# Kernel optimization log

Hardware: AMD Instinct MI355X
Metric: run time of the kernel (lower is better)

## Reference

```python
import jax, jax.numpy as jnp
import numpy as np

B, L, DM, H = 2, 2048, 1024, 16
D = DM // H  # head_dim = key_dim = 64


def setup_inputs() -> dict:
    key = jax.random.key(0)
    ks = jax.random.split(key, 6)
    w = 0.02
    return {
        "x": jax.random.normal(ks[0], (B, L, DM), dtype=jnp.float32),
        "wq_attn": jax.random.normal(ks[1], (DM, H * D), dtype=jnp.float32) * w,
        "wk_attn": jax.random.normal(ks[2], (DM, H * D), dtype=jnp.float32) * w,
        "wq_rel": jax.random.normal(ks[3], (DM, H * D), dtype=jnp.float32) * w,
        "wk_rel": jax.random.normal(ks[4], (DM, H * D), dtype=jnp.float32) * w,
        "wo": jax.random.normal(ks[5], (H * D, H * D), dtype=jnp.float32) * w,
    }


def reference(x, wq_attn, wk_attn, wq_rel, wk_rel, wo):
    b, l, dm = x.shape
    # projections -> (B, L, H, D); MHA so n_kv_heads == n_heads, no repeat_kv
    q = (x @ wq_attn).reshape(b, l, H, D)
    k = (x @ wk_attn).reshape(b, l, H, D)
    qr = (x @ wq_rel).reshape(b, l, H, D)
    kr = (x @ wk_rel).reshape(b, l, H, D)

    scale = D ** -0.5  # SDPA default: 1/sqrt(query key_dim)
    scores = jnp.einsum("blhd,bmhd->bhlm", q, k) * scale  # (B, H, L, L)
    causal = jnp.tril(jnp.ones((l, l), dtype=bool))
    scores = jnp.where(causal, scores, -jnp.inf)
    attn = jax.nn.softmax(scores, axis=-1)

    # attend over relational keys, then Hadamard with relational queries
    attended_kr = jnp.einsum("bhlm,bmhd->blhd", attn, kr)  # (B, L, H, D)
    attended_relations = qr * attended_kr                    # (B, L, H, D)

    out = attended_relations.reshape(b, l, H * D) @ wo       # (B, L, d_model)
    return out
```

## Files before the change

kernel.cpp:

```cpp
#include <hip/hip_runtime.h>
#include <stdint.h>


typedef __attribute__((ext_vector_type(4))) float floatx4;
typedef __attribute__((ext_vector_type(8))) short shortx8;
typedef __attribute__((ext_vector_type(4))) short shortx4;

__device__ __forceinline__ unsigned short f2bf(float f) {
    unsigned u = __float_as_uint(f);
    u += 0x7fffu + ((u >> 16) & 1u);
    return (unsigned short)(u >> 16);
}
__device__ __forceinline__ float bf2f(unsigned short s) {
    return __uint_as_float(((unsigned)s) << 16);
}
__device__ __forceinline__ float exp2fast(float x) {
#if __has_builtin(__builtin_amdgcn_exp2f)
    return __builtin_amdgcn_exp2f(x);
#else
    return __expf(x * 0.69314718056f);
#endif
}
__device__ __forceinline__ unsigned pkbf(float e0, float e1) {
    return __builtin_amdgcn_perm(__float_as_uint(e1), __float_as_uint(e0), 0x07060302u);
}
__device__ __forceinline__ floatx4 mfma16(shortx4 a, shortx4 b, floatx4 c) {
#if __has_builtin(__builtin_amdgcn_mfma_f32_16x16x16bf16_1k)
    return __builtin_amdgcn_mfma_f32_16x16x16bf16_1k(a, b, c, 0, 0, 0);
#else
    shortx8 a8 = {a[0], a[1], a[2], a[3], 0, 0, 0, 0};
    shortx8 b8 = {b[0], b[1], b[2], b[3], 0, 0, 0, 0};
    return __builtin_amdgcn_mfma_f32_16x16x32_bf16(a8, b8, c, 0, 0, 0);
#endif
}
__device__ __forceinline__ void gll16(const void* g, void* l) {
    __builtin_amdgcn_global_load_lds(
        (const __attribute__((address_space(1))) unsigned int*)g,
        (__attribute__((address_space(3))) unsigned int*)l, 16, 0, 0);
}

__global__ void k_cvt_x(const float* __restrict__ x, unsigned short* __restrict__ xb) {
    int i = (blockIdx.x * 256 + threadIdx.x) * 4;
    float4 v = *(const float4*)(x + i);
    ushort4 o;
    o.x = f2bf(v.x); o.y = f2bf(v.y); o.z = f2bf(v.z); o.w = f2bf(v.w);
    *(ushort4*)(xb + i) = o;
}

__global__ __launch_bounds__(256) void k_cvt_w5(const float* __restrict__ wq,
                                                const float* __restrict__ wk,
                                                const float* __restrict__ wqr,
                                                const float* __restrict__ wkr,
                                                const float* __restrict__ wo,
                                                unsigned short* __restrict__ wcatT,
                                                unsigned short* __restrict__ wotT) {
    __shared__ unsigned short Tl[64 * 65];
    const int t = threadIdx.x;
    const int kt = blockIdx.x * 64, nt = blockIdx.y * 64;
    const int z = blockIdx.z;
    const float* W = (z == 0) ? wq : (z == 1) ? wk : (z == 2) ? wqr : (z == 3) ? wkr : wo;
    unsigned short* outT = (z < 4) ? (wcatT + (size_t)z * 1024 * 1024) : wotT;
    const float scale = (z == 0) ? 0.18033688f : 1.0f;
    {
        const int kl = t >> 3, nc = (t & 7) * 8;
        const float* src = W + (size_t)(kt + kl) * 1024 + nt + nc;
        float a[8], b[8];
        *(float4*)(a)     = *(const float4*)(src);
        *(float4*)(a + 4) = *(const float4*)(src + 4);
        *(float4*)(b)     = *(const float4*)(src + 32 * 1024);
        *(float4*)(b + 4) = *(const float4*)(src + 32 * 1024 + 4);
#pragma unroll
        for (int i = 0; i < 8; ++i) {
            Tl[kl * 65 + nc + i]        = f2bf(a[i] * scale);
            Tl[(kl + 32) * 65 + nc + i] = f2bf(b[i] * scale);
        }
    }
    __syncthreads();
    {
        const int n = t >> 2, kc = (t & 3) * 16;
        shortx8 o0, o1;
#pragma unroll
        for (int i = 0; i < 8; ++i) {
            o0[i] = (short)Tl[(kc + i) * 65 + n];
            o1[i] = (short)Tl[(kc + 8 + i) * 65 + n];
        }
        unsigned short* dst = outT + (size_t)(nt + n) * 1024 + kt + kc;
        *(shortx8*)(dst)     = o0;
        *(shortx8*)(dst + 8) = o1;
    }
}

__global__ __launch_bounds__(512, 1) void k_gemm_bt256(const unsigned short* __restrict__ A,
                                                       const unsigned short* __restrict__ Bt,
                                                       unsigned short* __restrict__ C,
                                                       unsigned short* __restrict__ krT,
                                                       int K) {
    __shared__ alignas(16) unsigned short As[4][256 * 32];
    __shared__ alignas(16) unsigned short Bs[4][256 * 32];
    const int t = threadIdx.x;
    const int lane = t & 63, w = t >> 6;
    const int ln = lane & 15, quad = lane >> 4;
    const int wm = w >> 2, wn = w & 3;
    const int flat = blockIdx.x;
    const int xcd = flat & 7, idx = flat >> 3;
    const int bm = ((xcd >> 1) * 4 + (idx >> 3)) * 256;
    const int bn = ((xcd & 1) * 8 + (idx & 7)) * 256;

    floatx4 acc[8][4] = {};

    const int srow = t >> 2;
    const int sc = (t & 3) ^ ((srow >> 1) & 3);
    const unsigned short* gA = A + (size_t)(bm + srow) * K + sc * 8;
    const unsigned short* gB = Bt + (size_t)(bn + srow) * K + sc * 8;
    const int w16 = w * 16;

    auto stageA = [&](int kt, int buf) {
        const unsigned short* a = gA + (size_t)kt * 32;
        gll16(a,                   &As[buf][w16 * 32]);
        gll16(a + (size_t)128 * K, &As[buf][(128 + w16) * 32]);
    };
    auto stageB = [&](int kt, int buf) {
        const unsigned short* b = gB + (size_t)kt * 32;
        gll16(b,                   &Bs[buf][w16 * 32]);
        gll16(b + (size_t)128 * K, &Bs[buf][(128 + w16) * 32]);
    };

    const int NT = K >> 5;
    stageA(0, 0); stageB(0, 0);
    stageA(1, 1); stageB(1, 1);
    stageA(2, 2); stageB(2, 2);
    asm volatile("s_waitcnt vmcnt(8)" ::: "memory");
    __builtin_amdgcn_s_barrier();

    const int sw = (ln >> 1) & 3;
    for (int t0 = 0; t0 < NT; ++t0) {
        const unsigned short* Ab = As[t0 & 3];
        const unsigned short* Bb = Bs[t0 & 3];
        const int nb = (t0 + 3) & 3;
        shortx8 bfr0 = *(const shortx8*)(Bb + (wn * 64 + 0 * 16 + ln) * 32 + ((quad ^ sw) * 8));
        shortx8 bfr1 = *(const shortx8*)(Bb + (wn * 64 + 1 * 16 + ln) * 32 + ((quad ^ sw) * 8));
        shortx8 af[8];
#pragma unroll
        for (int i = 0; i < 8; ++i)
            af[i] = *(const shortx8*)(Ab + (wm * 128 + i * 16 + ln) * 32 + ((quad ^ sw) * 8));
        if (t0 + 3 < NT) stageA(t0 + 3, nb);
        asm volatile("" ::: "memory");
        __builtin_amdgcn_s_barrier();
        asm volatile("s_waitcnt lgkmcnt(0)" ::: "memory");
        __builtin_amdgcn_s_setprio(1);
#pragma unroll
        for (int i = 0; i < 8; ++i) {
            acc[i][0] = __builtin_amdgcn_mfma_f32_16x16x32_bf16(af[i], bfr0, acc[i][0], 0, 0, 0);
            acc[i][1] = __builtin_amdgcn_mfma_f32_16x16x32_bf16(af[i], bfr1, acc[i][1], 0, 0, 0);
        }
        __builtin_amdgcn_s_setprio(0);
        asm volatile("" ::: "memory");
        __builtin_amdgcn_s_barrier();
        shortx8 bfr2 = *(const shortx8*)(Bb + (wn * 64 + 2 * 16 + ln) * 32 + ((quad ^ sw) * 8));
        shortx8 bfr3 = *(const shortx8*)(Bb + (wn * 64 + 3 * 16 + ln) * 32 + ((quad ^ sw) * 8));
        if (t0 + 3 < NT) stageB(t0 + 3, nb);
        asm volatile("" ::: "memory");
        __builtin_amdgcn_s_barrier();
        asm volatile("s_waitcnt lgkmcnt(0)" ::: "memory");
        __builtin_amdgcn_s_setprio(1);
#pragma unroll
        for (int i = 0; i < 8; ++i) {
            acc[i][2] = __builtin_amdgcn_mfma_f32_16x16x32_bf16(af[i], bfr2, acc[i][2], 0, 0, 0);
            acc[i][3] = __builtin_amdgcn_mfma_f32_16x16x32_bf16(af[i], bfr3, acc[i][3], 0, 0, 0);
        }
        __builtin_amdgcn_s_setprio(0);
        if (t0 + 3 < NT) {
            asm volatile("s_waitcnt vmcnt(8)" ::: "memory");
        } else if (t0 + 2 < NT) {
            asm volatile("s_waitcnt vmcnt(4)" ::: "memory");
        } else if (t0 + 1 < NT) {
            asm volatile("s_waitcnt vmcnt(0)" ::: "memory");
        }
        asm volatile("" ::: "memory");
        __builtin_amdgcn_s_barrier();
    }

    if (bn < 3072) {
#pragma unroll
        for (int i = 0; i < 8; ++i)
#pragma unroll
            for (int j = 0; j < 4; ++j)
#pragma unroll
                for (int r = 0; r < 4; ++r) {
                    int row = bm + wm * 128 + i * 16 + quad * 4 + r;
                    int col = bn + wn * 64 + j * 16 + ln;
                    C[(size_t)row * 3072 + col] = f2bf(acc[i][j][r]);
                }
    } else {
        const int b = bm >> 11;
        const int l0b = (bm & 2047) + wm * 128 + quad * 4;
#pragma unroll
        for (int i = 0; i < 8; ++i)
#pragma unroll
            for (int j = 0; j < 4; ++j) {
                const int hd = (bn - 3072) + wn * 64 + j * 16 + ln;
                const int l0 = l0b + i * 16;
                shortx4 o;
#pragma unroll
                for (int r = 0; r < 4; ++r) o[r] = (short)f2bf(acc[i][j][r]);
                *(shortx4*)(krT + ((size_t)(b * 1024 + hd)) * 2048 + l0) = o;
            }
    }
}

__global__ __launch_bounds__(256) void k_gemm_n64(const unsigned short* __restrict__ A,
                                                  const unsigned short* __restrict__ Bt,
                                                  float* __restrict__ C,
                                                  int N, int K) {
    __shared__ alignas(16) unsigned short As[2][128 * 32];
    __shared__ alignas(16) unsigned short Bs[2][64 * 32];
    const int t = threadIdx.x;
    const int lane = t & 63, wv = t >> 6;
    const int ln = lane & 15, quad = lane >> 4;
    const int bm = blockIdx.y * 128, bn = blockIdx.x * 64;

    floatx4 acc[2][4] = {};

    const int srow = t >> 2;
    const int sc = (t & 3) ^ ((srow >> 1) & 3);
    const unsigned short* ga0 = A + (size_t)(bm + srow) * K + sc * 8;
    const unsigned short* ga1 = ga0 + (size_t)64 * K;
    const unsigned short* gb0 = Bt + (size_t)(bn + srow) * K + sc * 8;

    gll16(ga0, &As[0][wv * 512]);
    gll16(ga1, &As[0][2048 + wv * 512]);
    gll16(gb0, &Bs[0][wv * 512]);

    const int sw = (ln >> 1) & 3;
    int cur = 0;
    for (int k0 = 0; k0 < K; k0 += 32, cur ^= 1) {
        __syncthreads();
        const int nk = k0 + 32;
        if (nk < K) {
            gll16(ga0 + nk, &As[cur ^ 1][wv * 512]);
            gll16(ga1 + nk, &As[cur ^ 1][2048 + wv * 512]);
            gll16(gb0 + nk, &Bs[cur ^ 1][wv * 512]);
        }
        shortx8 af[2], bfr[4];
#pragma unroll
        for (int i = 0; i < 2; ++i)
            af[i] = *(const shortx8*)(&As[cur][(wv * 32 + i * 16 + ln) * 32 + ((quad ^ sw) * 8)]);
#pragma unroll
        for (int j = 0; j < 4; ++j)
            bfr[j] = *(const shortx8*)(&Bs[cur][(j * 16 + ln) * 32 + ((quad ^ sw) * 8)]);
#pragma unroll
        for (int i = 0; i < 2; ++i)
#pragma unroll
            for (int j = 0; j < 4; ++j)
                acc[i][j] = __builtin_amdgcn_mfma_f32_16x16x32_bf16(af[i], bfr[j], acc[i][j], 0, 0, 0);
    }

#pragma unroll
    for (int i = 0; i < 2; ++i)
#pragma unroll
        for (int j = 0; j < 4; ++j)
#pragma unroll
            for (int r = 0; r < 4; ++r) {
                int row = bm + wv * 32 + i * 16 + quad * 4 + r;
                int col = bn + j * 16 + ln;
                C[(size_t)row * N + col] = acc[i][j][r];
            }
}

__global__ __launch_bounds__(256, 2) void k_attn(const unsigned short* __restrict__ qcat,
                                                 const unsigned short* __restrict__ krT,
                                                 unsigned short* __restrict__ ar) {
    __shared__ alignas(16) unsigned short Kl[2][64 * 64];
    __shared__ alignas(16) unsigned short Rl[2][64 * 64];
    __shared__ float Ls[4][4][16];

    const int t = threadIdx.x;
    const int lane = t & 63, w = t >> 6;
    const int ln = lane & 15, quad = lane >> 4;
    const int flat = blockIdx.x;
    const int bh = (flat & 7) * 4 + ((flat >> 3) & 3);
    const int qts = flat >> 5;
    const int qt = (qts & 1) ? 31 - (qts >> 1) : (qts >> 1);
    const int b = bh >> 4, h = bh & 15;
    const int l0 = qt * 64;
    const size_t baserow = (size_t)b * 2048;

    shortx8 aq[4][2];
#pragma unroll
    for (int qc = 0; qc < 4; ++qc) {
        const unsigned short* qp =
            qcat + (baserow + l0 + qc * 16 + ln) * 3072 + h * 64 + quad * 8;
        aq[qc][0] = *(const shortx8*)(qp);
        aq[qc][1] = *(const shortx8*)(qp + 32);
    }

    floatx4 acc_o[4][4] = {};
    float lsum[4] = {0.f, 0.f, 0.f, 0.f};

    const int srow = t >> 3;
    const int sc = (t & 7) ^ (srow & 7);
    const unsigned short* gK = qcat + (baserow + srow) * 3072 + 1024 + h * 64 + sc * 8;
    const unsigned short* gR = krT + ((size_t)bh * 64 + srow) * 2048 + sc * 8;

    auto stage = [&](int kt, int buf) {
        gll16(gK + (size_t)(kt * 64) * 3072,      &Kl[buf][w * 512]);
        gll16(gK + (size_t)(kt * 64 + 32) * 3072, &Kl[buf][2048 + w * 512]);
        gll16(gR + kt * 64,                       &Rl[buf][w * 512]);
        gll16(gR + (size_t)32 * 2048 + kt * 64,   &Rl[buf][2048 + w * 512]);
    };

    stage(0, 0);
    const int swz = ln & 7;
    const int krow = (w * 16 + ln) * 64;
    const int cmw = w * 2 + (quad >> 1);
    int cur = 0;
    for (int kt = 0; kt <= qt; ++kt, cur ^= 1) {
        __syncthreads();
        if (kt < qt) stage(kt + 1, cur ^ 1);
        const unsigned short* Kc = Kl[cur];
        const unsigned short* Rc = Rl[cur];
        const bool diag = (kt == qt);

        shortx8 kf0 = *(const shortx8*)(Kc + krow + ((quad ^ swz) * 8));
        shortx8 kf1 = *(const shortx8*)(Kc + krow + (((4 + quad) ^ swz) * 8));
        shortx4 krf[4];
#pragma unroll
        for (int jd = 0; jd < 4; ++jd)
            krf[jd] = *(const shortx4*)(Rc + (jd * 16 + ln) * 64 +
                                        ((cmw ^ swz) * 8) + (quad & 1) * 4);

        const int keyb = kt * 64 + w * 16 + quad * 4;
        shortx4 pk[4];
#pragma unroll
        for (int qc = 0; qc < 4; ++qc) {
            floatx4 z = {0.f, 0.f, 0.f, 0.f};
            z = __builtin_amdgcn_mfma_f32_16x16x32_bf16(kf0, aq[qc][0], z, 0, 0, 0);
            z = __builtin_amdgcn_mfma_f32_16x16x32_bf16(kf1, aq[qc][1], z, 0, 0, 0);
            float e0 = exp2fast(z[0]);
            float e1 = exp2fast(z[1]);
            float e2 = exp2fast(z[2]);
            float e3 = exp2fast(z[3]);
            if (diag) {
                const int q = l0 + qc * 16 + ln;
                e0 = (keyb + 0 > q) ? 0.f : e0;
                e1 = (keyb + 1 > q) ? 0.f : e1;
                e2 = (keyb + 2 > q) ? 0.f : e2;
                e3 = (keyb + 3 > q) ? 0.f : e3;
            }
            lsum[qc] += (e0 + e1) + (e2 + e3);
            struct U2 { unsigned a, b; } u{pkbf(e0, e1), pkbf(e2, e3)};
            pk[qc] = __builtin_bit_cast(shortx4, u);
        }

        __builtin_amdgcn_s_setprio(1);
#pragma unroll
        for (int qc = 0; qc < 4; ++qc)
#pragma unroll
            for (int jd = 0; jd < 4; ++jd)
                acc_o[qc][jd] = mfma16(krf[jd], pk[qc], acc_o[qc][jd]);
        __builtin_amdgcn_s_setprio(0);
    }

#pragma unroll
    for (int qc = 0; qc < 4; ++qc) {
        float s = lsum[qc];
        s += __shfl_xor(s, 16);
        s += __shfl_xor(s, 32);
        lsum[qc] = s;
    }
    if (lane < 16) {
#pragma unroll
        for (int qc = 0; qc < 4; ++qc) Ls[w][qc][lane] = lsum[qc];
    }

    __syncthreads();
    float* redA = (float*)&Kl[0][0];
    float* redB = (float*)&Rl[0][0];
    if (w >= 2) {
        float* dst = (w == 2) ? redA : redB;
#pragma unroll
        for (int qc = 0; qc < 4; ++qc)
#pragma unroll
            for (int jd = 0; jd < 4; ++jd)
                *(floatx4*)(dst + ((qc * 4 + jd) * 64 + lane) * 4) = acc_o[qc][jd];
    }
    __syncthreads();
    if (w < 2) {
        const float* src = (w == 0) ? redA : redB;
#pragma unroll
        for (int qc = 0; qc < 4; ++qc)
#pragma unroll
            for (int jd = 0; jd < 4; ++jd)
                acc_o[qc][jd] += *(const floatx4*)(src + ((qc * 4 + jd) * 64 + lane) * 4);
    }
    __syncthreads();
    if (w == 1) {
#pragma unroll
        for (int qc = 0; qc < 4; ++qc)
#pragma unroll
            for (int jd = 0; jd < 4; ++jd)
                *(floatx4*)(redA + ((qc * 4 + jd) * 64 + lane) * 4) = acc_o[qc][jd];
    }
    __syncthreads();
    if (w == 0) {
        float inv[4];
#pragma unroll
        for (int qc = 0; qc < 4; ++qc)
            inv[qc] = 1.0f / (Ls[0][qc][ln] + Ls[1][qc][ln] + Ls[2][qc][ln] + Ls[3][qc][ln]);
#pragma unroll
        for (int qc = 0; qc < 4; ++qc) {
            const int q = l0 + qc * 16 + ln;
            const unsigned short* qr = qcat + (baserow + q) * 3072 + 2048 + h * 64;
            unsigned short* arow = ar + (baserow + q) * 1024 + h * 64;
#pragma unroll
            for (int jd = 0; jd < 4; ++jd) {
                floatx4 a = acc_o[qc][jd];
                a += *(const floatx4*)(redA + ((qc * 4 + jd) * 64 + lane) * 4);
                const int d0 = jd * 16 + quad * 4;
                shortx4 qv = *(const shortx4*)(qr + d0);
                shortx4 o;
#pragma unroll
                for (int r = 0; r < 4; ++r)
                    o[r] = (short)f2bf(a[r] * inv[qc] * bf2f((unsigned short)qv[r]));
                *(shortx4*)(arow + d0) = o;
            }
        }
    }
}

extern "C" void kernel_launch(void* const* d_in, const int* in_sizes, int n_in,
                              void* d_out, int out_size, void* d_ws, size_t ws_size,
                              hipStream_t stream) {
    const float* x   = (const float*)d_in[0];
    const float* wq  = (const float*)d_in[1];
    const float* wk  = (const float*)d_in[2];
    const float* wqr = (const float*)d_in[3];
    const float* wkr = (const float*)d_in[4];
    const float* wo  = (const float*)d_in[5];
    float* out = (float*)d_out;

    unsigned short* xb    = (unsigned short*)d_ws;
    unsigned short* wcatT = xb + (size_t)4096 * 1024;
    unsigned short* qcat  = wcatT + (size_t)4096 * 1024;
    unsigned short* krT   = qcat + (size_t)4096 * 3072;
    unsigned short* wotT  = krT + (size_t)32 * 64 * 2048;
    unsigned short* arb   = xb;

    k_cvt_x<<<4096, 256, 0, stream>>>(x, xb);
    k_cvt_w5<<<dim3(16, 16, 5), 256, 0, stream>>>(wq, wk, wqr, wkr, wo, wcatT, wotT);
    k_gemm_bt256<<<256, 512, 0, stream>>>(xb, wcatT, qcat, krT, 1024);
    k_attn<<<1024, 256, 0, stream>>>(qcat, krT, arb);
    k_gemm_n64<<<dim3(16, 32), 256, 0, stream>>>(arb, wotT, out, 1024, 1024);
}
```

Measured before the change: 184.0 us.

## Deepen GEMM K-tile to 64 with double buffering and finer-grained staged prefetch

The projection GEMM's LDS tiles go from four 256x32 buffers to two 256x64 buffers. Each K-step now issues twice as many MFMAs per barrier phase, and global-to-LDS loads are split into quarter-tile stages interleaved across eight compute phases with explicit vmcnt waits. The XOR swizzle is widened to 8 chunks to match the 64-wide rows. The goal is to cut per-K-step barrier and LDS-read overhead relative to MFMA work. The trade-off is a shallower prefetch distance and hand-tuned wait counts, which are easy to get wrong.

```diff
diff --git a/kernel.cpp b/kernel.cpp
--- a/kernel.cpp
+++ b/kernel.cpp
@@ -95,8 +95,8 @@
                                                        unsigned short* __restrict__ C,
                                                        unsigned short* __restrict__ krT,
                                                        int K) {
-    __shared__ alignas(16) unsigned short As[4][256 * 32];
-    __shared__ alignas(16) unsigned short Bs[4][256 * 32];
+    __shared__ alignas(16) unsigned short As[2][256 * 64];
+    __shared__ alignas(16) unsigned short Bs[2][256 * 64];
     const int t = threadIdx.x;
     const int lane = t & 63, w = t >> 6;
     const int ln = lane & 15, quad = lane >> 4;
@@ -107,78 +107,86 @@
     const int bn = ((xcd & 1) * 8 + (idx & 7)) * 256;
 
     floatx4 acc[8][4] = {};
-
-    const int srow = t >> 2;
-    const int sc = (t & 3) ^ ((srow >> 1) & 3);
-    const unsigned short* gA = A + (size_t)(bm + srow) * K + sc * 8;
-    const unsigned short* gB = Bt + (size_t)(bn + srow) * K + sc * 8;
-    const int w16 = w * 16;
-
-    auto stageA = [&](int kt, int buf) {
-        const unsigned short* a = gA + (size_t)kt * 32;
-        gll16(a,                   &As[buf][w16 * 32]);
-        gll16(a + (size_t)128 * K, &As[buf][(128 + w16) * 32]);
+    shortx8 bfr[4][2];
+
+    const int srow8 = w * 8 + (lane >> 3);
+    const int sc8 = (lane & 7) ^ (lane >> 3);
+    const unsigned short* gA2 = A + (size_t)(bm + srow8) * K + sc8 * 8;
+    const unsigned short* gB2 = Bt + (size_t)(bn + srow8) * K + sc8 * 8;
+    const int wb = w * 512;
+
+    auto stA = [&](int kt, int c, int qr) {
+        const unsigned short* s = gA2 + (size_t)(qr * 64) * K + kt * 64;
+        gll16(s,                   &As[c][(qr * 64) * 64 + wb]);
+        gll16(s + (size_t)128 * K, &As[c][(128 + qr * 64) * 64 + wb]);
     };
-    auto stageB = [&](int kt, int buf) {
-        const unsigned short* b = gB + (size_t)kt * 32;
-        gll16(b,                   &Bs[buf][w16 * 32]);
-        gll16(b + (size_t)128 * K, &Bs[buf][(128 + w16) * 32]);
+    auto stB = [&](int kt, int c, int h) {
+        const unsigned short* s = gB2 + (size_t)(h * 128) * K + kt * 64;
+        gll16(s,                  &Bs[c][(h * 128) * 64 + wb]);
+        gll16(s + (size_t)64 * K, &Bs[c][(h * 128 + 64) * 64 + wb]);
     };
 
-    const int NT = K >> 5;
-    stageA(0, 0); stageB(0, 0);
-    stageA(1, 1); stageB(1, 1);
-    stageA(2, 2); stageB(2, 2);
+    stB(0, 0, 0); stB(0, 0, 1); stA(0, 0, 0); stA(0, 0, 1);
+    stB(1, 1, 0); stB(1, 1, 1); stA(1, 1, 0);
     asm volatile("s_waitcnt vmcnt(8)" ::: "memory");
     __builtin_amdgcn_s_barrier();
 
-    const int sw = (ln >> 1) & 3;
-    for (int t0 = 0; t0 < NT; ++t0) {
-        const unsigned short* Ab = As[t0 & 3];
-        const unsigned short* Bb = Bs[t0 & 3];
-        const int nb = (t0 + 3) & 3;
-        shortx8 bfr0 = *(const shortx8*)(Bb + (wn * 64 + 0 * 16 + ln) * 32 + ((quad ^ sw) * 8));
-        shortx8 bfr1 = *(const shortx8*)(Bb + (wn * 64 + 1 * 16 + ln) * 32 + ((quad ^ sw) * 8));
-        shortx8 af[8];
-#pragma unroll
-        for (int i = 0; i < 8; ++i)
-            af[i] = *(const shortx8*)(Ab + (wm * 128 + i * 16 + ln) * 32 + ((quad ^ sw) * 8));
-        if (t0 + 3 < NT) stageA(t0 + 3, nb);
-        asm volatile("" ::: "memory");
-        __builtin_amdgcn_s_barrier();
-        asm volatile("s_waitcnt lgkmcnt(0)" ::: "memory");
-        __builtin_amdgcn_s_setprio(1);
-#pragma unroll
-        for (int i = 0; i < 8; ++i) {
-            acc[i][0] = __builtin_amdgcn_mfma_f32_16x16x32_bf16(af[i], bfr0, acc[i][0], 0, 0, 0);
-            acc[i][1] = __builtin_amdgcn_mfma_f32_16x16x32_bf16(af[i], bfr1, acc[i][1], 0, 0, 0);
-        }
-        __builtin_amdgcn_s_setprio(0);
-        asm volatile("" ::: "memory");
-        __builtin_amdgcn_s_barrier();
-        shortx8 bfr2 = *(const shortx8*)(Bb + (wn * 64 + 2 * 16 + ln) * 32 + ((quad ^ sw) * 8));
-        shortx8 bfr3 = *(const shortx8*)(Bb + (wn * 64 + 3 * 16 + ln) * 32 + ((quad ^ sw) * 8));
-        if (t0 + 3 < NT) stageB(t0 + 3, nb);
-        asm volatile("" ::: "memory");
-        __builtin_amdgcn_s_barrier();
-        asm volatile("s_waitcnt lgkmcnt(0)" ::: "memory");
-        __builtin_amdgcn_s_setprio(1);
-#pragma unroll
-        for (int i = 0; i < 8; ++i) {
-            acc[i][2] = __builtin_amdgcn_mfma_f32_16x16x32_bf16(af[i], bfr2, acc[i][2], 0, 0, 0);
-            acc[i][3] = __builtin_amdgcn_mfma_f32_16x16x32_bf16(af[i], bfr3, acc[i][3], 0, 0, 0);
-        }
-        __builtin_amdgcn_s_setprio(0);
-        if (t0 + 3 < NT) {
-            asm volatile("s_waitcnt vmcnt(8)" ::: "memory");
-        } else if (t0 + 2 < NT) {
-            asm volatile("s_waitcnt vmcnt(4)" ::: "memory");
-        } else if (t0 + 1 < NT) {
-            asm volatile("s_waitcnt vmcnt(0)" ::: "memory");
-        }
-        asm volatile("" ::: "memory");
-        __builtin_amdgcn_s_barrier();
-    }
+    const int sl0 = (quad ^ (ln & 7)) * 8;
+    const int sl1 = ((4 + quad) ^ (ln & 7)) * 8;
+
+#define GVM(n_) asm volatile("s_waitcnt vmcnt(" #n_ ")" ::: "memory")
+#define GLDB(c_)                                                              \
+    {                                                                         \
+        _Pragma("unroll")                                                     \
+        for (int j = 0; j < 4; ++j) {                                         \
+            const int br_ = (wn * 64 + j * 16 + ln) * 64;                     \
+            bfr[j][0] = *(const shortx8*)(&Bs[c_][br_ + sl0]);                \
+            bfr[j][1] = *(const shortx8*)(&Bs[c_][br_ + sl1]);                \
+        }                                                                     \
+    }
+#define GPH(c_, q_, STAGE_STMT, VM_STMT)                                      \
+    {                                                                         \
+        const int rb_ = (wm * 128 + (q_) * 32 + ln) * 64;                     \
+        shortx8 af00 = *(const shortx8*)(&As[c_][rb_ + sl0]);                 \
+        shortx8 af01 = *(const shortx8*)(&As[c_][rb_ + sl1]);                 \
+        shortx8 af10 = *(const shortx8*)(&As[c_][rb_ + 1024 + sl0]);          \
+        shortx8 af11 = *(const shortx8*)(&As[c_][rb_ + 1024 + sl1]);          \
+        STAGE_STMT                                                            \
+        asm volatile("" ::: "memory");                                        \
+        __builtin_amdgcn_s_barrier();                                         \
+        asm volatile("s_waitcnt lgkmcnt(0)" ::: "memory");                    \
+        __builtin_amdgcn_s_setprio(1);                                        \
+        _Pragma("unroll")                                                     \
+        for (int j = 0; j < 4; ++j) {                                         \
+            acc[(q_)*2][j]   = __builtin_amdgcn_mfma_f32_16x16x32_bf16(af00, bfr[j][0], acc[(q_)*2][j], 0, 0, 0);   \
+            acc[(q_)*2][j]   = __builtin_amdgcn_mfma_f32_16x16x32_bf16(af01, bfr[j][1], acc[(q_)*2][j], 0, 0, 0);   \
+            acc[(q_)*2+1][j] = __builtin_amdgcn_mfma_f32_16x16x32_bf16(af10, bfr[j][0], acc[(q_)*2+1][j], 0, 0, 0); \
+            acc[(q_)*2+1][j] = __builtin_amdgcn_mfma_f32_16x16x32_bf16(af11, bfr[j][1], acc[(q_)*2+1][j], 0, 0, 0); \
+        }                                                                     \
+        __builtin_amdgcn_s_setprio(0);                                        \
+        VM_STMT                                                               \
+        asm volatile("" ::: "memory");                                        \
+        __builtin_amdgcn_s_barrier();                                         \
+    }
+
+    const int NI = K >> 7;
+    for (int I = 0; I < NI; ++I) {
+        const int n = 2 * I;
+        const bool L = (I == NI - 1);
+        GLDB(0)
+        GPH(0, 0, { stA(n + 1, 1, 1); }, {})
+        GPH(0, 1, { if (!L) stB(n + 2, 0, 0); }, { if (L) { GVM(8); } else { GVM(10); } })
+        GPH(0, 2, { if (!L) stB(n + 2, 0, 1); }, {})
+        GPH(0, 3, { if (!L) stA(n + 2, 0, 0); }, { if (L) { GVM(2); } else { GVM(8); } })
+        GLDB(1)
+        GPH(1, 0, { if (!L) stA(n + 2, 0, 1); }, {})
+        GPH(1, 1, { if (!L) stB(n + 3, 1, 0); }, { if (L) { GVM(0); } else { GVM(10); } })
+        GPH(1, 2, { if (!L) stB(n + 3, 1, 1); }, {})
+        GPH(1, 3, { if (!L) stA(n + 3, 1, 0); }, { if (!L) { GVM(8); } })
+    }
+#undef GPH
+#undef GLDB
+#undef GVM
 
     if (bn < 3072) {
 #pragma unroll
```

Result: no change. 181.7 us (median of 2 runs) (-1.3%).
